# Performance work log

Hardware: AMD Instinct MI355X
Metric: run time of the kernel (lower is better)

## Reference

```python
import jax, jax.numpy as jnp
import numpy as np

P = 920   # spatial positions per frame (hard-coded in source)
FRAMES = 5
H = 8     # num_heads
C = 256   # dim


def setup_inputs() -> dict:
    key = jax.random.key(0)
    ks = jax.random.split(key, 6)
    B = 4
    s = 0.02
    return {
        "x": jax.random.normal(ks[0], (P, B * FRAMES, C), dtype=jnp.float32),
        "W_qkv": jax.random.normal(ks[1], (3 * C, C), dtype=jnp.float32) * s,
        "W_pq": jax.random.normal(ks[2], (C, C), dtype=jnp.float32) * s,
        "W_pkv": jax.random.normal(ks[3], (2 * C, C), dtype=jnp.float32) * s,
        "W_proj": jax.random.normal(ks[4], (C, C), dtype=jnp.float32) * s,
        "b_proj": jnp.zeros((C,), dtype=jnp.float32),
    }


def reference(x, W_qkv, W_pq, W_pkv, W_proj, b_proj):
    d = C // H
    scale = d ** -0.5
    N = FRAMES * P

    # (P, B*F, C) -> (B*F, P, C) -> (B, F*P, C)
    xb = jnp.transpose(x, (1, 0, 2)).reshape(-1, N, C)
    B = xb.shape[0]

    # Stage 1: space attention (note: heads are NOT split here, per original code)
    qkv = xb @ W_qkv.T                      # (B, N, 3C)
    q_, k_, v_ = jnp.split(qkv, 3, axis=-1)
    q_dot_k = jnp.einsum('bqc,bnc->bqn', q_, k_)        # (B, N, N)
    q_dot_k = q_dot_k.reshape(B, N, FRAMES, P)          # b q f n
    space_attn = jax.nn.softmax(scale * q_dot_k, axis=-1)
    v_f = v_.reshape(B, FRAMES, P, C)                   # b f n d
    x1 = jnp.einsum('bqfn,bfnd->bqfd', space_attn, v_f)  # (B, N, F, C)

    # Diagonal extraction: each spatial position attends to its own frame
    xg = x1.reshape(B, FRAMES, P, FRAMES, C)            # b g n f d
    x_diag = jnp.diagonal(xg, axis1=1, axis2=3)         # (B, P, C, F)
    x_diag = jnp.transpose(x_diag, (0, 3, 1, 2)).reshape(B, N, C)  # b (f n) d

    # Stage 2: trajectory attention over frames, with heads
    q2 = x_diag @ W_pq.T                                # (B, N, C)
    kv2 = x1 @ W_pkv.T                                  # (B, N, F, 2C)
    k2, v2 = jnp.split(kv2, 2, axis=-1)
    q2 = q2.reshape(B, N, H, d).transpose(0, 2, 1, 3) * scale      # b h s d
    k2 = k2.reshape(B, N, FRAMES, H, d).transpose(0, 3, 1, 2, 4)   # b h s f d
    v2 = v2.reshape(B, N, FRAMES, H, d).transpose(0, 3, 1, 2, 4)
    attn = jax.nn.softmax(jnp.einsum('bhsd,bhsfd->bhsf', q2, k2), axis=-1)
    x2 = jnp.einsum('bhsf,bhsfd->bhsd', attn, v2)       # (B, H, N, d)
    x2 = x2.transpose(0, 2, 1, 3).reshape(B, N, C)

    out = x2 @ W_proj.T + b_proj                        # (B, N, C)
    out = out.reshape(B, FRAMES, P, C).reshape(B * FRAMES, P, C)
    out = jnp.transpose(out, (1, 0, 2))                 # (P, B*F, C)
    return out, attn
```

## Files before the change

kernel.cpp:

```cpp
#include <hip/hip_runtime.h>
#include <stdint.h>

#define PP 920
#define FF 5
#define BBATCH 4
#define CC 256
#define NN 4600
#define HH 8
#define MROWS 18400
#define M2ROWS 92000
#define SCALE 0.17677669529663687f


typedef short bf16x8 __attribute__((ext_vector_type(8)));
typedef float f32x4 __attribute__((ext_vector_type(4)));
typedef float f32x16 __attribute__((ext_vector_type(16)));
typedef uint32_t u32;

#define MFMA16 __builtin_amdgcn_mfma_f32_16x16x32_bf16
#define MFMA32 __builtin_amdgcn_mfma_f32_32x32x16_bf16

__device__ __forceinline__ float b2f(unsigned short s){
  u32 u = ((u32)s) << 16; float f; __builtin_memcpy(&f, &u, 4); return f;
}
__device__ __forceinline__ unsigned short f2b(float f){
  u32 u; __builtin_memcpy(&u, &f, 4);
  u = (u + 0x7FFFu + ((u >> 16) & 1u)) >> 16;
  return (unsigned short)u;
}


__global__ void k16_cast(const float* __restrict__ in, short* __restrict__ out, int n){
  int i = blockIdx.x*256 + threadIdx.x;
  if (i < n) out[i] = (short)f2b(in[i]);
}

__global__ void k16_make_xb(const float* __restrict__ x, short* __restrict__ xb){
  int i = blockIdx.x*256 + threadIdx.x;
  long e0 = (long)i*4;
  if (e0 >= (long)MROWS*CC) return;
  int row = (int)(e0 >> 8); int c = (int)(e0 & 255);
  int b = row / NN; int s = row - b*NN; int f = s / PP; int p = s - f*PP;
  const float4 v = *(const float4*)(x + ((size_t)(p*(BBATCH*FF) + b*FF + f))*CC + c);
  unsigned short o[4];
  o[0]=f2b(v.x); o[1]=f2b(v.y); o[2]=f2b(v.z); o[3]=f2b(v.w);
  *(ushort4*)(xb + e0) = *(ushort4*)o;
}

__global__ void k16_zero(short* p, int n){
  int i = blockIdx.x*256 + threadIdx.x;
  if (i < n) p[i] = 0;
}

template<int MODE>
__launch_bounds__(256)
__global__ void k16_gemm(const short* __restrict__ A, const short* __restrict__ Bw,
                         short* __restrict__ Cout, float* __restrict__ FCout,
                         const float* __restrict__ bias,
                         int M, int lda, int ldc, float alpha)
{
  __shared__ short As[128][40];
  __shared__ short Bs[128][40];
  const int tid = threadIdx.x;
  const int m0 = blockIdx.x*128, n0 = blockIdx.y*128;
  const int w = tid >> 6, l = tid & 63;
  const int wm = (w >> 1)*64, wn = (w & 1)*64;
  const int lr = l & 15, lg = l >> 4;

  f32x4 acc[4][4] = {};

  for (int k0 = 0; k0 < 256; k0 += 32){
    #pragma unroll
    for (int i = 0; i < 2; i++){
      int v = tid + 256*i;
      int ar = v >> 2, as = (v & 3)*8;
      int grow = m0 + ar; if (grow >= M) grow = M - 1;
      *(uint4*)(&As[ar][as]) = *(const uint4*)(A + (size_t)grow*lda + k0 + as);
      *(uint4*)(&Bs[ar][as]) = *(const uint4*)(Bw + (size_t)(n0 + ar)*256 + k0 + as);
    }
    __syncthreads();
    bf16x8 af[4], bfr[4];
    #pragma unroll
    for (int i = 0; i < 4; i++) af[i]  = *(const bf16x8*)(&As[wm + i*16 + lr][lg*8]);
    #pragma unroll
    for (int j = 0; j < 4; j++) bfr[j] = *(const bf16x8*)(&Bs[wn + j*16 + lr][lg*8]);
    #pragma unroll
    for (int i = 0; i < 4; i++)
      #pragma unroll
      for (int j = 0; j < 4; j++)
        acc[i][j] = MFMA16(af[i], bfr[j], acc[i][j], 0, 0, 0);
    __syncthreads();
  }

  #pragma unroll
  for (int i = 0; i < 4; i++){
    #pragma unroll
    for (int r = 0; r < 4; r++){
      int m = m0 + wm + i*16 + lg*4 + r;
      if (m >= M) continue;
      #pragma unroll
      for (int j = 0; j < 4; j++){
        int n = n0 + wn + j*16 + lr;
        float v = acc[i][j][r]*alpha;
        if (MODE == 1){
          v += bias[n];
          int b = m / NN, s = m - b*NN; int f = s / PP, p = s - f*PP;
          FCout[(size_t)(p*(BBATCH*FF) + b*FF + f)*CC + n] = v;
        } else {
          Cout[(size_t)m*ldc + n] = (short)f2b(v);
        }
      }
    }
  }
}

__launch_bounds__(256)
__global__ void k16_vt(const short* __restrict__ qkv, short* __restrict__ vt){
  __shared__ short t[64][80];
  const int p0 = blockIdx.x*64;
  const int c0 = blockIdx.y*64;
  const int bf = blockIdx.z;
  const int b = bf / FF, f = bf - b*FF;
  const int tid = threadIdx.x;
  #pragma unroll
  for (int i = 0; i < 2; i++){
    int v = tid + 256*i;
    int pr = v >> 3, sg = (v & 7)*8;
    uint4 val = make_uint4(0,0,0,0);
    int p = p0 + pr;
    if (p < PP)
      val = *(const uint4*)(qkv + ((size_t)(b*NN + f*PP + p))*768 + 512 + c0 + sg);
    *(uint4*)(&t[pr][sg]) = val;
  }
  __syncthreads();
  #pragma unroll
  for (int i = 0; i < 2; i++){
    int v = tid + 256*i;
    int cr = v & 63, pg = v >> 6;
    int pbase = p0 + pg*8;
    if (pbase < 928){
      unsigned short o[8];
      #pragma unroll
      for (int jj = 0; jj < 8; jj++) o[jj] = (unsigned short)t[pg*8 + jj][cr];
      *(uint4*)(vt + ((size_t)(bf*CC + c0 + cr))*928 + pbase) = *(uint4*)o;
    }
  }
}

__launch_bounds__(256)
__global__ void k16_flash(const short* __restrict__ qkv, const short* __restrict__ vt,
                          short* __restrict__ x1, short* __restrict__ xd)
{
  __shared__ short Ks[32][264];
  __shared__ short Vs[256][40];
  __shared__ short Ps[4][32][40];

  const int qt = blockIdx.x, f = blockIdx.y, b = blockIdx.z;
  const int tid = threadIdx.x, w = tid >> 6, l = tid & 63;
  const int cl = l & 31, hi = l >> 5;
  const int qbase = qt*128 + w*32;

  bf16x8 qa[16];
  {
    int qrow = qbase + cl; if (qrow > NN - 1) qrow = NN - 1;
    const short* qp = qkv + (size_t)(b*NN + qrow)*768 + hi*8;
    #pragma unroll
    for (int kk = 0; kk < 16; kk++) qa[kk] = *(const bf16x8*)(qp + kk*16);
  }

  f32x16 o[8] = {};
  float den[16] = {};

  const size_t krow0 = (size_t)(b*NN + f*PP)*768 + 256;
  const short* vtp = vt + (size_t)((b*FF + f)*CC)*928;

  for (int ch = 0; ch < 29; ch++){
    const int key0 = ch*32;
    #pragma unroll
    for (int i = 0; i < 4; i++){
      int v = tid + 256*i;
      int kr = v >> 5, ks = (v & 31)*8;
      *(uint4*)(&Ks[kr][ks]) = *(const uint4*)(qkv + krow0 + (size_t)(key0 + kr)*768 + ks);
    }
    {
      const short* vp = vtp + (size_t)tid*928 + key0;
      #pragma unroll
      for (int i = 0; i < 4; i++)
        *(uint4*)(&Vs[tid][i*8]) = *(const uint4*)(vp + i*8);
    }
    __syncthreads();

    f32x16 s = {};
    #pragma unroll
    for (int kk = 0; kk < 16; kk++){
      bf16x8 kb = *(const bf16x8*)(&Ks[cl][kk*16 + hi*8]);
      s = MFMA32(qa[kk], kb, s, 0, 0, 0);
    }

    const bool valid = (key0 + cl) < PP;
    #pragma unroll
    for (int r = 0; r < 16; r++){
      float v = valid ? s[r]*SCALE : -1e30f;
      float p = __expf(v);
      den[r] += p;
      int qr = (r & 3) + 8*(r >> 2) + 4*hi;
      Ps[w][qr][cl] = (short)f2b(p);
    }

    bf16x8 pa0 = *(const bf16x8*)(&Ps[w][cl][hi*8]);
    bf16x8 pa1 = *(const bf16x8*)(&Ps[w][cl][16 + hi*8]);
    #pragma unroll
    for (int ct = 0; ct < 8; ct++){
      bf16x8 vb0 = *(const bf16x8*)(&Vs[ct*32 + cl][hi*8]);
      bf16x8 vb1 = *(const bf16x8*)(&Vs[ct*32 + cl][16 + hi*8]);
      o[ct] = MFMA32(pa0, vb0, o[ct], 0, 0, 0);
      o[ct] = MFMA32(pa1, vb1, o[ct], 0, 0, 0);
    }
    __syncthreads();
  }

  #pragma unroll
  for (int r = 0; r < 16; r++){
    float dsum = den[r];
    #pragma unroll
    for (int off = 16; off >= 1; off >>= 1) dsum += __shfl_xor(dsum, off);
    float inv = 1.f/dsum;
    int srow = qbase + (r & 3) + 8*(r >> 2) + 4*hi;
    if (srow >= NN) continue;
    bool dg = (srow/PP == f);
    size_t x1base = ((size_t)(b*NN + srow)*FF + f)*CC;
    size_t xdbase = (size_t)(b*NN + srow)*CC;
    #pragma unroll
    for (int ct = 0; ct < 8; ct++){
      short val = (short)f2b(o[ct][r]*inv);
      x1[x1base + ct*32 + cl] = val;
      if (dg) xd[xdbase + ct*32 + cl] = val;
    }
  }
}

__launch_bounds__(256)
__global__ void k16_attn2(const short* __restrict__ q2b, const short* __restrict__ k2v2,
                          float* __restrict__ attnp, short* __restrict__ x2)
{
  int idx = blockIdx.x*256 + threadIdx.x;
  if (idx >= MROWS*HH) return;
  const int h = idx & 7; const int row = idx >> 3;

  float qv[32];
  {
    const short* qp = q2b + (size_t)row*CC + h*32;
    #pragma unroll
    for (int s4 = 0; s4 < 4; s4++){
      uint4 u = *(const uint4*)(qp + s4*8);
      const unsigned short* sp = (const unsigned short*)&u;
      #pragma unroll
      for (int j = 0; j < 8; j++) qv[s4*8 + j] = b2f(sp[j]);
    }
  }

  float lgt[FF];
  #pragma unroll
  for (int f = 0; f < FF; f++){
    const short* kp = k2v2 + ((size_t)row*FF + f)*512 + h*32;
    float a = 0.f;
    #pragma unroll
    for (int s4 = 0; s4 < 4; s4++){
      uint4 u = *(const uint4*)(kp + s4*8);
      const unsigned short* sp = (const unsigned short*)&u;
      #pragma unroll
      for (int j = 0; j < 8; j++) a += qv[s4*8 + j]*b2f(sp[j]);
    }
    lgt[f] = a;
  }

  float mx = lgt[0];
  #pragma unroll
  for (int f = 1; f < FF; f++) mx = fmaxf(mx, lgt[f]);
  float pr[FF], ps = 0.f;
  #pragma unroll
  for (int f = 0; f < FF; f++){ pr[f] = __expf(lgt[f] - mx); ps += pr[f]; }
  float inv = 1.f/ps;

  const int b = row / NN; const int s = row - b*NN;
  size_t ab = (((size_t)(b*HH + h))*NN + s)*FF;
  #pragma unroll
  for (int f = 0; f < FF; f++) attnp[ab + f] = pr[f]*inv;

  float xa[32] = {};
  #pragma unroll
  for (int f = 0; f < FF; f++){
    const short* vp = k2v2 + ((size_t)row*FF + f)*512 + 256 + h*32;
    float wgt = pr[f]*inv;
    #pragma unroll
    for (int s4 = 0; s4 < 4; s4++){
      uint4 u = *(const uint4*)(vp + s4*8);
      const unsigned short* sp = (const unsigned short*)&u;
      #pragma unroll
      for (int j = 0; j < 8; j++) xa[s4*8 + j] += wgt*b2f(sp[j]);
    }
  }
  #pragma unroll
  for (int s4 = 0; s4 < 4; s4++){
    unsigned short o[8];
    #pragma unroll
    for (int j = 0; j < 8; j++) o[j] = f2b(xa[s4*8 + j]);
    *(uint4*)(x2 + (size_t)row*CC + h*32 + s4*8) = *(uint4*)o;
  }
}

extern "C" void kernel_launch(void* const* d_in, const int* in_sizes, int n_in,
                              void* d_out, int out_size, void* d_ws, size_t ws_size,
                              hipStream_t stream)
{
  int ix=-1, iwqkv=-1, iwpq=-1, iwpkv=-1, iwproj=-1, ib=-1;
  for (int i = 0; i < n_in; i++){
    switch (in_sizes[i]){
      case 4710400: ix = i; break;
      case 196608:  iwqkv = i; break;
      case 131072:  iwpkv = i; break;
      case 256:     ib = i; break;
      case 65536:   if (iwpq < 0) iwpq = i; else iwproj = i; break;
      default: break;
    }
  }
  if (ix < 0 || iwqkv < 0 || iwpq < 0 || iwpkv < 0 || iwproj < 0 || ib < 0){
    ix=0; iwqkv=1; iwpq=2; iwpkv=3; iwproj=4; ib=5;
  }
  const float* x     = (const float*)d_in[ix];
  const float* Wqkv  = (const float*)d_in[iwqkv];
  const float* Wpq   = (const float*)d_in[iwpq];
  const float* Wpkv  = (const float*)d_in[iwpkv];
  const float* Wproj = (const float*)d_in[iwproj];
  const float* bproj = (const float*)d_in[ib];

  char* ws = (char*)d_ws;
  if (ws_size < 208269312ULL) return;

  short* wq    = (short*)(ws + 0);
  short* wpq   = (short*)(ws + 393216);
  short* wpkv  = (short*)(ws + 524288);
  short* wprj  = (short*)(ws + 786432);
  short* xb    = (short*)(ws + 917504);
  short* qkv   = (short*)(ws + 10338304);
  short* vt    = (short*)(ws + 38612992);
  short* x1    = (short*)(ws + 48115712);
  short* xd    = (short*)(ws + 95219712);
  short* k2v2  = (short*)(ws + 104640512);
  short* q2b   = (short*)(ws + 198848512);
  short* x2    = xb;

  float* outp  = (float*)d_out;
  float* attnp = outp + 4710400;

  k16_cast<<<dim3(768), dim3(256), 0, stream>>>(Wqkv,  wq,   196608);
  k16_cast<<<dim3(256), dim3(256), 0, stream>>>(Wpq,   wpq,  65536);
  k16_cast<<<dim3(512), dim3(256), 0, stream>>>(Wpkv,  wpkv, 131072);
  k16_cast<<<dim3(256), dim3(256), 0, stream>>>(Wproj, wprj, 65536);
  k16_make_xb<<<dim3(4600), dim3(256), 0, stream>>>(x, xb);
  k16_zero<<<dim3(24), dim3(256), 0, stream>>>(qkv + (size_t)MROWS*768, 6144);

  k16_gemm<0><<<dim3(144, 6), dim3(256), 0, stream>>>(xb, wq, qkv, nullptr, nullptr, MROWS, 256, 768, 1.0f);
  k16_vt<<<dim3(15, 4, 20), dim3(256), 0, stream>>>(qkv, vt);
  k16_flash<<<dim3(36, 5, 4), dim3(256), 0, stream>>>(qkv, vt, x1, xd);
  k16_gemm<0><<<dim3(719, 4), dim3(256), 0, stream>>>(x1, wpkv, k2v2, nullptr, nullptr, M2ROWS, 256, 512, 1.0f);
  k16_gemm<0><<<dim3(144, 2), dim3(256), 0, stream>>>(xd, wpq, q2b, nullptr, nullptr, MROWS, 256, 256, SCALE);
  k16_attn2<<<dim3(575), dim3(256), 0, stream>>>(q2b, k2v2, attnp, x2);
  k16_gemm<1><<<dim3(144, 2), dim3(256), 0, stream>>>(x2, wprj, nullptr, outp, bproj, MROWS, 256, 256, 1.0f);
}
```

Baseline: 353.9 us.

## Double-buffer K/V tiles and keep softmax probabilities in registers in flash kernel

```diff
diff --git a/kernel.cpp b/kernel.cpp
--- a/kernel.cpp
+++ b/kernel.cpp
@@ -30,12 +30,12 @@
 }
 
 
-__global__ void k16_cast(const float* __restrict__ in, short* __restrict__ out, int n){
+__global__ void k17_cast(const float* __restrict__ in, short* __restrict__ out, int n){
   int i = blockIdx.x*256 + threadIdx.x;
   if (i < n) out[i] = (short)f2b(in[i]);
 }
 
-__global__ void k16_make_xb(const float* __restrict__ x, short* __restrict__ xb){
+__global__ void k17_make_xb(const float* __restrict__ x, short* __restrict__ xb){
   int i = blockIdx.x*256 + threadIdx.x;
   long e0 = (long)i*4;
   if (e0 >= (long)MROWS*CC) return;
@@ -47,14 +47,14 @@
   *(ushort4*)(xb + e0) = *(ushort4*)o;
 }
 
-__global__ void k16_zero(short* p, int n){
+__global__ void k17_zero(short* p, int n){
   int i = blockIdx.x*256 + threadIdx.x;
   if (i < n) p[i] = 0;
 }
 
 template<int MODE>
 __launch_bounds__(256)
-__global__ void k16_gemm(const short* __restrict__ A, const short* __restrict__ Bw,
+__global__ void k17_gemm(const short* __restrict__ A, const short* __restrict__ Bw,
                          short* __restrict__ Cout, float* __restrict__ FCout,
                          const float* __restrict__ bias,
                          int M, int lda, int ldc, float alpha)
@@ -115,7 +115,7 @@
 }
 
 __launch_bounds__(256)
-__global__ void k16_vt(const short* __restrict__ qkv, short* __restrict__ vt){
+__global__ void k17_vt(const short* __restrict__ qkv, short* __restrict__ vt){
   __shared__ short t[64][80];
   const int p0 = blockIdx.x*64;
   const int c0 = blockIdx.y*64;
@@ -148,15 +148,15 @@
 }
 
 __launch_bounds__(256)
-__global__ void k16_flash(const short* __restrict__ qkv, const short* __restrict__ vt,
+__global__ void k17_flash(const short* __restrict__ qkv, const short* __restrict__ vt,
                           short* __restrict__ x1, short* __restrict__ xd)
 {
-  __shared__ short Ks[32][264];
-  __shared__ short Vs[256][40];
-  __shared__ short Ps[4][32][40];
+  __shared__ short Ks[2][32][264];
+  __shared__ short Vs[2][256][40];
 
   const int qt = blockIdx.x, f = blockIdx.y, b = blockIdx.z;
-  const int tid = threadIdx.x, w = tid >> 6, l = tid & 63;
+  const int tid = threadIdx.x, l = tid & 63;
+  const int w = tid >> 6;
   const int cl = l & 31, hi = l >> 5;
   const int qbase = qt*128 + w*32;
 
@@ -169,63 +169,99 @@
   }
 
   f32x16 o[8] = {};
-  float den[16] = {};
+  float den = 0.f;
 
   const size_t krow0 = (size_t)(b*NN + f*PP)*768 + 256;
   const short* vtp = vt + (size_t)((b*FF + f)*CC)*928;
 
-  for (int ch = 0; ch < 29; ch++){
+  uint4 kreg[4], vreg[4];
+  const int skr = tid >> 5;
+
+  auto stage_load = [&](int ch){
     const int key0 = ch*32;
     #pragma unroll
     for (int i = 0; i < 4; i++){
       int v = tid + 256*i;
       int kr = v >> 5, ks = (v & 31)*8;
-      *(uint4*)(&Ks[kr][ks]) = *(const uint4*)(qkv + krow0 + (size_t)(key0 + kr)*768 + ks);
-    }
-    {
-      const short* vp = vtp + (size_t)tid*928 + key0;
-      #pragma unroll
-      for (int i = 0; i < 4; i++)
-        *(uint4*)(&Vs[tid][i*8]) = *(const uint4*)(vp + i*8);
-    }
+      kreg[i] = *(const uint4*)(qkv + krow0 + (size_t)(key0 + kr)*768 + ks);
+    }
+    const short* vp = vtp + (size_t)tid*928 + key0;
+    #pragma unroll
+    for (int i = 0; i < 4; i++) vreg[i] = *(const uint4*)(vp + i*8);
+  };
+  auto stage_write = [&](int buf){
+    #pragma unroll
+    for (int i = 0; i < 4; i++){
+      int v = tid + 256*i;
+      int kr = v >> 5, ks = (v & 31)*8;
+      *(uint4*)(&Ks[buf][kr][ks]) = kreg[i];
+    }
+    #pragma unroll
+    for (int i = 0; i < 4; i++) *(uint4*)(&Vs[buf][tid][i*8]) = vreg[i];
+  };
+
+  stage_load(0);
+  stage_write(0);
+
+  for (int ch = 0; ch < 29; ch++){
+    const int cur = ch & 1;
+    const int key0 = ch*32;
     __syncthreads();
 
+    if (ch < 28) stage_load(ch + 1);
+
     f32x16 s = {};
     #pragma unroll
     for (int kk = 0; kk < 16; kk++){
-      bf16x8 kb = *(const bf16x8*)(&Ks[cl][kk*16 + hi*8]);
-      s = MFMA32(qa[kk], kb, s, 0, 0, 0);
-    }
-
-    const bool valid = (key0 + cl) < PP;
+      bf16x8 kb = *(const bf16x8*)(&Ks[cur][cl][kk*16 + hi*8]);
+      s = MFMA32(kb, qa[kk], s, 0, 0, 0);
+    }
+
+    float p[16];
     #pragma unroll
     for (int r = 0; r < 16; r++){
-      float v = valid ? s[r]*SCALE : -1e30f;
-      float p = __expf(v);
-      den[r] += p;
-      int qr = (r & 3) + 8*(r >> 2) + 4*hi;
-      Ps[w][qr][cl] = (short)f2b(p);
-    }
-
-    bf16x8 pa0 = *(const bf16x8*)(&Ps[w][cl][hi*8]);
-    bf16x8 pa1 = *(const bf16x8*)(&Ps[w][cl][16 + hi*8]);
+      int key = key0 + (r & 3) + 8*(r >> 2) + 4*hi;
+      float v = (key < PP) ? s[r]*SCALE : -1e30f;
+      p[r] = __expf(v);
+      den += p[r];
+    }
+
+    u32 u0 = (u32)f2b(p[0])  | ((u32)f2b(p[1])  << 16);
+    u32 u1 = (u32)f2b(p[2])  | ((u32)f2b(p[3])  << 16);
+    u32 u2 = (u32)f2b(p[4])  | ((u32)f2b(p[5])  << 16);
+    u32 u3 = (u32)f2b(p[6])  | ((u32)f2b(p[7])  << 16);
+    u32 u4 = (u32)f2b(p[8])  | ((u32)f2b(p[9])  << 16);
+    u32 u5 = (u32)f2b(p[10]) | ((u32)f2b(p[11]) << 16);
+    u32 u6 = (u32)f2b(p[12]) | ((u32)f2b(p[13]) << 16);
+    u32 u7 = (u32)f2b(p[14]) | ((u32)f2b(p[15]) << 16);
+    asm("v_permlane32_swap_b32 %0, %1" : "+v"(u0), "+v"(u2));
+    asm("v_permlane32_swap_b32 %0, %1" : "+v"(u1), "+v"(u3));
+    asm("v_permlane32_swap_b32 %0, %1" : "+v"(u4), "+v"(u6));
+    asm("v_permlane32_swap_b32 %0, %1" : "+v"(u5), "+v"(u7));
+    u32 f1[4] = {u0, u1, u2, u3};
+    u32 f2[4] = {u4, u5, u6, u7};
+    bf16x8 pa0, pa1;
+    __builtin_memcpy(&pa0, f1, 16);
+    __builtin_memcpy(&pa1, f2, 16);
+
     #pragma unroll
     for (int ct = 0; ct < 8; ct++){
-      bf16x8 vb0 = *(const bf16x8*)(&Vs[ct*32 + cl][hi*8]);
-      bf16x8 vb1 = *(const bf16x8*)(&Vs[ct*32 + cl][16 + hi*8]);
+      bf16x8 vb0 = *(const bf16x8*)(&Vs[cur][ct*32 + cl][hi*8]);
+      bf16x8 vb1 = *(const bf16x8*)(&Vs[cur][ct*32 + cl][16 + hi*8]);
       o[ct] = MFMA32(pa0, vb0, o[ct], 0, 0, 0);
       o[ct] = MFMA32(pa1, vb1, o[ct], 0, 0, 0);
     }
-    __syncthreads();
-  }
-
+
+    if (ch < 28) stage_write(cur ^ 1);
+  }
+
+  den += __shfl_xor(den, 32);
+  float invd = 1.f/den;
   #pragma unroll
   for (int r = 0; r < 16; r++){
-    float dsum = den[r];
-    #pragma unroll
-    for (int off = 16; off >= 1; off >>= 1) dsum += __shfl_xor(dsum, off);
-    float inv = 1.f/dsum;
-    int srow = qbase + (r & 3) + 8*(r >> 2) + 4*hi;
+    int qr = (r & 3) + 8*(r >> 2) + 4*hi;
+    float inv = __shfl(invd, qr);
+    int srow = qbase + qr;
     if (srow >= NN) continue;
     bool dg = (srow/PP == f);
     size_t x1base = ((size_t)(b*NN + srow)*FF + f)*CC;
@@ -240,7 +276,7 @@
 }
 
 __launch_bounds__(256)
-__global__ void k16_attn2(const short* __restrict__ q2b, const short* __restrict__ k2v2,
+__global__ void k17_attn2(const short* __restrict__ q2b, const short* __restrict__ k2v2,
                           float* __restrict__ attnp, short* __restrict__ x2)
 {
   int idx = blockIdx.x*256 + threadIdx.x;
@@ -353,18 +389,18 @@
   float* outp  = (float*)d_out;
   float* attnp = outp + 4710400;
 
-  k16_cast<<<dim3(768), dim3(256), 0, stream>>>(Wqkv,  wq,   196608);
-  k16_cast<<<dim3(256), dim3(256), 0, stream>>>(Wpq,   wpq,  65536);
-  k16_cast<<<dim3(512), dim3(256), 0, stream>>>(Wpkv,  wpkv, 131072);
-  k16_cast<<<dim3(256), dim3(256), 0, stream>>>(Wproj, wprj, 65536);
-  k16_make_xb<<<dim3(4600), dim3(256), 0, stream>>>(x, xb);
-  k16_zero<<<dim3(24), dim3(256), 0, stream>>>(qkv + (size_t)MROWS*768, 6144);
-
-  k16_gemm<0><<<dim3(144, 6), dim3(256), 0, stream>>>(xb, wq, qkv, nullptr, nullptr, MROWS, 256, 768, 1.0f);
-  k16_vt<<<dim3(15, 4, 20), dim3(256), 0, stream>>>(qkv, vt);
-  k16_flash<<<dim3(36, 5, 4), dim3(256), 0, stream>>>(qkv, vt, x1, xd);
-  k16_gemm<0><<<dim3(719, 4), dim3(256), 0, stream>>>(x1, wpkv, k2v2, nullptr, nullptr, M2ROWS, 256, 512, 1.0f);
-  k16_gemm<0><<<dim3(144, 2), dim3(256), 0, stream>>>(xd, wpq, q2b, nullptr, nullptr, MROWS, 256, 256, SCALE);
-  k16_attn2<<<dim3(575), dim3(256), 0, stream>>>(q2b, k2v2, attnp, x2);
-  k16_gemm<1><<<dim3(144, 2), dim3(256), 0, stream>>>(x2, wprj, nullptr, outp, bproj, MROWS, 256, 256, 1.0f);
-}
+  k17_cast<<<dim3(768), dim3(256), 0, stream>>>(Wqkv,  wq,   196608);
+  k17_cast<<<dim3(256), dim3(256), 0, stream>>>(Wpq,   wpq,  65536);
+  k17_cast<<<dim3(512), dim3(256), 0, stream>>>(Wpkv,  wpkv, 131072);
+  k17_cast<<<dim3(256), dim3(256), 0, stream>>>(Wproj, wprj, 65536);
+  k17_make_xb<<<dim3(4600), dim3(256), 0, stream>>>(x, xb);
+  k17_zero<<<dim3(24), dim3(256), 0, stream>>>(qkv + (size_t)MROWS*768, 6144);
+
+  k17_gemm<0><<<dim3(144, 6), dim3(256), 0, stream>>>(xb, wq, qkv, nullptr, nullptr, MROWS, 256, 768, 1.0f);
+  k17_vt<<<dim3(15, 4, 20), dim3(256), 0, stream>>>(qkv, vt);
+  k17_flash<<<dim3(36, 5, 4), dim3(256), 0, stream>>>(qkv, vt, x1, xd);
+  k17_gemm<0><<<dim3(719, 4), dim3(256), 0, stream>>>(x1, wpkv, k2v2, nullptr, nullptr, M2ROWS, 256, 512, 1.0f);
+  k17_gemm<0><<<dim3(144, 2), dim3(256), 0, stream>>>(xd, wpq, q2b, nullptr, nullptr, MROWS, 256, 256, SCALE);
+  k17_attn2<<<dim3(575), dim3(256), 0, stream>>>(q2b, k2v2, attnp, x2);
+  k17_gemm<1><<<dim3(144, 2), dim3(256), 0, stream>>>(x2, wprj, nullptr, outp, bproj, MROWS, 256, 256, 1.0f);
+}
```

Result: slower. 527.4 us (+49.0%).
